# Performance work log

Measured on AMD Instinct MI355X. Metric: run time of the kernel, lower is better.

Reference implementation:

```python
import jax, jax.numpy as jnp
import numpy as np

B, S = 128, 32
V, E, H, L = 32000, 512, 1024, 2


def setup_inputs() -> dict:
    key = jax.random.key(0)
    ks = jax.random.split(key, 16)
    s = 0.02  # weight scale
    inp = {
        "x": jax.random.randint(ks[0], (B, S), 0, V),
        "encoder_output": jax.random.normal(ks[1], (S, B, H), jnp.float32),  # unused by module
        "encoder_hidden_state": jax.random.normal(ks[2], (L, B, H), jnp.float32),
        "emb": jax.random.normal(ks[3], (V, E), jnp.float32) * s,
        "w_ih0": jax.random.normal(ks[4], (3 * H, E), jnp.float32) * s,
        "w_hh0": jax.random.normal(ks[5], (3 * H, H), jnp.float32) * s,
        "b_ih0": jax.random.normal(ks[6], (3 * H,), jnp.float32) * s,
        "b_hh0": jax.random.normal(ks[7], (3 * H,), jnp.float32) * s,
        "w_ih1": jax.random.normal(ks[8], (3 * H, H), jnp.float32) * s,
        "w_hh1": jax.random.normal(ks[9], (3 * H, H), jnp.float32) * s,
        "b_ih1": jax.random.normal(ks[10], (3 * H,), jnp.float32) * s,
        "b_hh1": jax.random.normal(ks[11], (3 * H,), jnp.float32) * s,
        "w_dec": jax.random.normal(ks[12], (V, H), jnp.float32) * s,
        "b_dec": jax.random.normal(ks[13], (V,), jnp.float32) * s,
        "max_seq_length": S,
    }
    return inp


def _gru_cell(h, xt, w_ih, w_hh, b_ih, b_hh):
    # PyTorch GRU gate math
    gi = xt @ w_ih.T + b_ih  # [B, 3H]
    gh = h @ w_hh.T + b_hh   # [B, 3H]
    ir, iz, inn = jnp.split(gi, 3, axis=-1)
    hr, hz, hn = jnp.split(gh, 3, axis=-1)
    r = jax.nn.sigmoid(ir + hr)
    z = jax.nn.sigmoid(iz + hz)
    n = jnp.tanh(inn + r * hn)
    return (1.0 - z) * n + z * h


def reference(x, encoder_output, encoder_hidden_state, emb,
              w_ih0, w_hh0, b_ih0, b_hh0,
              w_ih1, w_hh1, b_ih1, b_hh1,
              w_dec, b_dec, max_seq_length):
    # teaching_rate = 0.0 -> pure teacher forcing; dropout p=0.0 -> identity.
    # Step 0 consumes SOS token (id 1, from torch.ones().long()); steps 1..T-1 consume x[:, i].
    Bsz = x.shape[0]
    sos = jnp.ones((Bsz, 1), jnp.int32)
    toks = jnp.concatenate([sos, x[:, 1:max_seq_length].astype(jnp.int32)], axis=1)  # [B, T]
    xs = emb[toks].transpose(1, 0, 2)  # [T, B, E] (seq-first, matching permute(1,0,2))

    def step(carry, xt):
        h0, h1 = carry
        h0 = _gru_cell(h0, xt, w_ih0, w_hh0, b_ih0, b_hh0)
        h1 = _gru_cell(h1, h0, w_ih1, w_hh1, b_ih1, b_hh1)
        return (h0, h1), h1

    init = (encoder_hidden_state[0], encoder_hidden_state[1])
    _, ys = jax.lax.scan(step, init, xs)  # ys: [T, B, H]
    logits = jnp.einsum('tbh,vh->tbv', ys, w_dec) + b_dec  # [T, B, V]
    return logits
```

## Files before the change

kernel.cpp:

```cpp
#include <hip/hip_runtime.h>
#include <hip/hip_bf16.h>
#include <stdint.h>

#define T_SEQ 32
#define BATCH 128
#define EMB   512
#define HID   1024
#define VOC   32000
#define G3    (3 * HID)
#define MROWS (T_SEQ * BATCH)
#define BHID  (BATCH * HID)

typedef __bf16 bf16_t;
typedef __bf16 bf16x8 __attribute__((ext_vector_type(8)));
typedef __bf16 bf16x4 __attribute__((ext_vector_type(4)));
typedef float  f32x4  __attribute__((ext_vector_type(4)));

#define MFMA(a, b, c) __builtin_amdgcn_mfma_f32_16x16x32_bf16((a), (b), (c), 0, 0, 0)

union U64cast  { bf16x4 v; unsigned long long u; };
union U128cast { f32x4 v; unsigned long long u[2]; };

__device__ __forceinline__ unsigned flag_ld(const unsigned* p) {
    return __hip_atomic_load(p, __ATOMIC_RELAXED, __HIP_MEMORY_SCOPE_SYSTEM);
}
__device__ __forceinline__ void flag_st(unsigned* p, unsigned v) {
    __hip_atomic_store(p, v, __ATOMIC_RELAXED, __HIP_MEMORY_SCOPE_SYSTEM);
}

__global__ void fused_cvt_kernel(
    const float* __restrict__ w_ih0, const float* __restrict__ w_hh0,
    const float* __restrict__ w_ih1, const float* __restrict__ w_hh1,
    const float* __restrict__ w_dec, const float* __restrict__ enc_hid,
    bf16_t* __restrict__ Wih0b, bf16_t* __restrict__ Whh0b,
    bf16_t* __restrict__ Wih1b, bf16_t* __restrict__ Whh1b,
    bf16_t* __restrict__ Wdecb, bf16_t* __restrict__ h0ib,
    bf16_t* __restrict__ h1ib) {
    const int b = blockIdx.x;
    const float* src;
    bf16_t* dst;
    int base;
    if (b < 1536)       { src = w_ih0;          dst = Wih0b; base = b; }
    else if (b < 4608)  { src = w_hh0;          dst = Whh0b; base = b - 1536; }
    else if (b < 7680)  { src = w_ih1;          dst = Wih1b; base = b - 4608; }
    else if (b < 10752) { src = w_hh1;          dst = Whh1b; base = b - 7680; }
    else if (b < 42752) { src = w_dec;          dst = Wdecb; base = b - 10752; }
    else if (b < 42880) { src = enc_hid;        dst = h0ib;  base = b - 42752; }
    else                { src = enc_hid + BHID; dst = h1ib;  base = b - 42880; }
    const int i = base * 1024 + threadIdx.x * 4;
    float4 v = *(const float4*)(src + i);
    dst[i + 0] = (bf16_t)v.x;
    dst[i + 1] = (bf16_t)v.y;
    dst[i + 2] = (bf16_t)v.z;
    dst[i + 3] = (bf16_t)v.w;
}

__global__ void embed_kernel(const int* __restrict__ x,
                             const float* __restrict__ emb,
                             bf16_t* __restrict__ X) {
    int m = blockIdx.x;
    int t = m >> 7, b = m & 127;
    int tok = (t == 0) ? 1 : x[b * T_SEQ + t];
    const float* src = emb + (size_t)tok * EMB;
    bf16_t* dst = X + (size_t)m * EMB;
    int c = threadIdx.x * 4;
    float4 v = *(const float4*)(src + c);
    dst[c + 0] = (bf16_t)v.x;
    dst[c + 1] = (bf16_t)v.y;
    dst[c + 2] = (bf16_t)v.z;
    dst[c + 3] = (bf16_t)v.w;
}

#define GLOAD_LDS16(g, l)                                                    \
    __builtin_amdgcn_global_load_lds(                                        \
        (const __attribute__((address_space(1))) void*)(g),                  \
        (__attribute__((address_space(3))) void*)(l), 16, 0, 0)

template <int BIAS>
__global__ __launch_bounds__(256) void gemm_bf16_kernel(
    const bf16_t* __restrict__ A, const bf16_t* __restrict__ B,
    const float* __restrict__ bias, float* __restrict__ C,
    int M, int N, int K) {
    __shared__ __align__(16) bf16_t As[128 * 32];
    __shared__ __align__(16) bf16_t Bs[128 * 32];

    const int nbm = gridDim.y, nbn = gridDim.x;
    const int nwg = nbm * nbn;
    int lin = blockIdx.y * nbn + blockIdx.x;
    if ((nwg & 7) == 0) {
        int xcd = lin & 7, idx = lin >> 3;
        lin = xcd * (nwg >> 3) + idx;
    }
    const int bm = (lin % nbm) * 128;
    const int bn = (lin / nbm) * 128;

    const int tid  = threadIdx.x;
    const int lane = tid & 63;
    const int w    = tid >> 6;
    const int wr   = w >> 1, wc = w & 1;

    f32x4 acc[4][4] = {};

    const int lrow = tid >> 2;
    const int lcol = (tid & 3) * 8;
    const bf16_t* ag = A + (size_t)(bm + lrow) * K + lcol;
    const bf16_t* bg = B + (size_t)(bn + lrow) * K + lcol;
    bf16_t* asl0 = As + lrow * 32 + lcol;
    bf16_t* asl1 = As + (lrow + 64) * 32 + lcol;
    bf16_t* bsl0 = Bs + lrow * 32 + lcol;
    bf16_t* bsl1 = Bs + (lrow + 64) * 32 + lcol;

    const int r16 = lane & 15;
    const int kh  = (lane >> 4) * 8;

    for (int k0 = 0; k0 < K; k0 += 32) {
        GLOAD_LDS16(ag + k0, asl0);
        GLOAD_LDS16(ag + (size_t)64 * K + k0, asl1);
        GLOAD_LDS16(bg + k0, bsl0);
        GLOAD_LDS16(bg + (size_t)64 * K + k0, bsl1);
        __syncthreads();

        bf16x8 af[4], bf[4];
#pragma unroll
        for (int mi = 0; mi < 4; ++mi)
            af[mi] = *(const bf16x8*)(As + (wr * 64 + mi * 16 + r16) * 32 + kh);
#pragma unroll
        for (int ni = 0; ni < 4; ++ni)
            bf[ni] = *(const bf16x8*)(Bs + (wc * 64 + ni * 16 + r16) * 32 + kh);
#pragma unroll
        for (int mi = 0; mi < 4; ++mi)
#pragma unroll
            for (int ni = 0; ni < 4; ++ni)
                acc[mi][ni] = MFMA(af[mi], bf[ni], acc[mi][ni]);
        __syncthreads();
    }

#pragma unroll
    for (int mi = 0; mi < 4; ++mi) {
        const int row0 = bm + wr * 64 + mi * 16 + (lane >> 4) * 4;
#pragma unroll
        for (int ni = 0; ni < 4; ++ni) {
            const int col = bn + wc * 64 + ni * 16 + r16;
            float bv = 0.f;
            if (BIAS) bv = bias[col];
#pragma unroll
            for (int r = 0; r < 4; ++r)
                C[(size_t)(row0 + r) * N + col] = acc[mi][ni][r] + bv;
        }
    }
}

template <int BIAS>
__global__ __launch_bounds__(512, 1) void gemm256_bf16_kernel(
    const bf16_t* __restrict__ A, const bf16_t* __restrict__ B,
    const float* __restrict__ bias, float* __restrict__ C,
    int M, int N, int K) {
    __shared__ __align__(16) bf16_t lds[2 * 2 * 16384];

    const int NT = K >> 6;
    const int nbm = gridDim.y, nbn = gridDim.x;
    const int nwg = nbm * nbn;
    int lin = blockIdx.y * nbn + blockIdx.x;
    {
        int q = nwg >> 3, r = nwg & 7, x = lin & 7, i = lin >> 3;
        lin = (x < r ? x * (q + 1) : r * (q + 1) + (x - r) * q) + i;
    }
    const int bm = (lin % nbm) * 256;
    const int bn = (lin / nbm) * 256;

    const int tid = threadIdx.x, lane = tid & 63;
    const int w = tid >> 6, wm = w >> 2, wn = w & 3;
    const int r16 = lane & 15, sl = lane >> 4, r7 = r16 & 7;

    const int srow  = tid >> 3;
    const int sslot = (tid & 7) ^ (srow & 7);
    const bf16_t* agS = A + (size_t)(bm + srow) * K + sslot * 8;
    const bf16_t* bgS = B + (size_t)(bn + srow) * K + sslot * 8;

    const int colk0 = ((0 + sl) ^ r7) * 8;
    const int colk1 = ((4 + sl) ^ r7) * 8;
    const int arow = (wm * 128 + r16) * 64;
    const int brow = (wn * 64 + r16) * 64;

    f32x4 acc[8][4] = {};
    bf16x8 af[4][2], bf[4][2];

#pragma unroll
    for (int l = 0; l < 4; ++l)
        GLOAD_LDS16(agS + (size_t)(l * 64) * K, lds + l * 4096 + tid * 8);
#pragma unroll
    for (int l = 0; l < 4; ++l)
        GLOAD_LDS16(bgS + (size_t)(l * 64) * K, lds + 16384 + l * 4096 + tid * 8);
#pragma unroll
    for (int l = 0; l < 4; ++l)
        GLOAD_LDS16(agS + (size_t)(l * 64) * K + 64,
                    lds + 32768 + l * 4096 + tid * 8);
#pragma unroll
    for (int l = 0; l < 4; ++l)
        GLOAD_LDS16(bgS + (size_t)(l * 64) * K + 64,
                    lds + 49152 + l * 4096 + tid * 8);
    asm volatile("s_waitcnt vmcnt(8)" ::: "memory");
    __builtin_amdgcn_sched_barrier(0);
    __builtin_amdgcn_s_barrier();

#pragma unroll 1
    for (int kt = 0; kt < NT; ++kt) {
        const int cur = kt & 1;
        const bf16_t* Ab = lds + cur * 32768;
        const bf16_t* Bb = Ab + 16384;
        bf16_t* Sb = lds + cur * 32768;
        const bool st = (kt + 2 < NT);
        const size_t kof = (size_t)(kt + 2) * 64;

#pragma unroll
        for (int fr = 0; fr < 4; ++fr) {
            af[fr][0] = *(const bf16x8*)(Ab + arow + fr * 1024 + colk0);
            af[fr][1] = *(const bf16x8*)(Ab + arow + fr * 1024 + colk1);
        }
#pragma unroll
        for (int nf = 0; nf < 2; ++nf) {
            bf[nf][0] = *(const bf16x8*)(Bb + brow + nf * 1024 + colk0);
            bf[nf][1] = *(const bf16x8*)(Bb + brow + nf * 1024 + colk1);
        }
        __builtin_amdgcn_sched_barrier(0);
        __builtin_amdgcn_s_barrier();
        asm volatile("s_waitcnt lgkmcnt(0)" ::: "memory");
        __builtin_amdgcn_sched_barrier(0);
        __builtin_amdgcn_s_setprio(1);
#pragma unroll
        for (int fr = 0; fr < 4; ++fr)
#pragma unroll
            for (int nf = 0; nf < 2; ++nf) {
                acc[fr][nf] = MFMA(af[fr][0], bf[nf][0], acc[fr][nf]);
                acc[fr][nf] = MFMA(af[fr][1], bf[nf][1], acc[fr][nf]);
            }
        __builtin_amdgcn_s_setprio(0);
        __builtin_amdgcn_sched_barrier(0);
        __builtin_amdgcn_s_barrier();

#pragma unroll
        for (int nf = 2; nf < 4; ++nf) {
            bf[nf][0] = *(const bf16x8*)(Bb + brow + nf * 1024 + colk0);
            bf[nf][1] = *(const bf16x8*)(Bb + brow + nf * 1024 + colk1);
        }
        __builtin_amdgcn_sched_barrier(0);
        if (st) {
            GLOAD_LDS16(agS + kof, Sb + tid * 8);
            GLOAD_LDS16(agS + (size_t)128 * K + kof, Sb + 8192 + tid * 8);
        }
        __builtin_amdgcn_s_barrier();
        asm volatile("s_waitcnt lgkmcnt(0)" ::: "memory");
        __builtin_amdgcn_sched_barrier(0);
        __builtin_amdgcn_s_setprio(1);
#pragma unroll
        for (int fr = 0; fr < 4; ++fr)
#pragma unroll
            for (int nf = 2; nf < 4; ++nf) {
                acc[fr][nf] = MFMA(af[fr][0], bf[nf][0], acc[fr][nf]);
                acc[fr][nf] = MFMA(af[fr][1], bf[nf][1], acc[fr][nf]);
            }
        __builtin_amdgcn_s_setprio(0);
        __builtin_amdgcn_sched_barrier(0);
        __builtin_amdgcn_s_barrier();

#pragma unroll
        for (int fr = 0; fr < 4; ++fr) {
            af[fr][0] = *(const bf16x8*)(Ab + arow + (fr + 4) * 1024 + colk0);
            af[fr][1] = *(const bf16x8*)(Ab + arow + (fr + 4) * 1024 + colk1);
        }
        __builtin_amdgcn_sched_barrier(0);
        if (st) {
#pragma unroll
            for (int l = 0; l < 4; ++l)
                GLOAD_LDS16(bgS + (size_t)(l * 64) * K + kof,
                            Sb + 16384 + l * 4096 + tid * 8);
        }
        __builtin_amdgcn_s_barrier();
        asm volatile("s_waitcnt lgkmcnt(0)" ::: "memory");
        __builtin_amdgcn_sched_barrier(0);
        __builtin_amdgcn_s_setprio(1);
#pragma unroll
        for (int fr = 0; fr < 4; ++fr)
#pragma unroll
            for (int nf = 0; nf < 2; ++nf) {
                acc[fr + 4][nf] = MFMA(af[fr][0], bf[nf][0], acc[fr + 4][nf]);
                acc[fr + 4][nf] = MFMA(af[fr][1], bf[nf][1], acc[fr + 4][nf]);
            }
        __builtin_amdgcn_s_setprio(0);
        __builtin_amdgcn_sched_barrier(0);
        __builtin_amdgcn_s_barrier();

        if (st) {
            GLOAD_LDS16(agS + (size_t)64 * K + kof, Sb + 4096 + tid * 8);
            GLOAD_LDS16(agS + (size_t)192 * K + kof, Sb + 12288 + tid * 8);
        }
        if (kt + 2 < NT) {
            asm volatile("s_waitcnt vmcnt(8)" ::: "memory");
        } else if (kt + 1 < NT) {
            asm volatile("s_waitcnt vmcnt(0)" ::: "memory");
        }
        __builtin_amdgcn_sched_barrier(0);
        __builtin_amdgcn_s_setprio(1);
#pragma unroll
        for (int fr = 0; fr < 4; ++fr)
#pragma unroll
            for (int nf = 2; nf < 4; ++nf) {
                acc[fr + 4][nf] = MFMA(af[fr][0], bf[nf][0], acc[fr + 4][nf]);
                acc[fr + 4][nf] = MFMA(af[fr][1], bf[nf][1], acc[fr + 4][nf]);
            }
        __builtin_amdgcn_s_setprio(0);
        __builtin_amdgcn_sched_barrier(0);
        __builtin_amdgcn_s_barrier();
    }

#pragma unroll
    for (int fr = 0; fr < 8; ++fr) {
        const int row0 = bm + wm * 128 + fr * 16 + sl * 4;
#pragma unroll
        for (int nf = 0; nf < 4; ++nf) {
            const int col = bn + wn * 64 + nf * 16 + r16;
            float bv = 0.f;
            if (BIAS) bv = bias[col];
#pragma unroll
            for (int r = 0; r < 4; ++r)
                __builtin_nontemporal_store(
                    acc[fr][nf][r] + bv, &C[(size_t)(row0 + r) * N + col]);
        }
    }
}

__global__ __launch_bounds__(256, 1) void fused_scan_kernel(
    const bf16_t* __restrict__ h0ib, const bf16_t* __restrict__ h1ib,
    const float* __restrict__ enc_hid,
    const bf16_t* __restrict__ whh0, const bf16_t* __restrict__ wih1,
    const bf16_t* __restrict__ whh1,
    const float* __restrict__ bhh0, const float* __restrict__ bih1,
    const float* __restrict__ bhh1,
    float* __restrict__ Gi, bf16_t* __restrict__ H0b,
    bf16_t* __restrict__ H1b, unsigned* __restrict__ wfl) {
    __shared__ __align__(16) float Sg[4][3][128][16];

    const int tid  = threadIdx.x;
    const int lane = tid & 63;
    const int w    = tid >> 6;
    const int role = blockIdx.x >> 6;
    const int cb   = blockIdx.x & 63;
    const int c0   = cb * 16;
    const int r16  = lane & 15;
    const int kq   = (lane >> 4) * 8;

    const int FL0 = 0, FG = 256, FL1 = 512;

    const bf16_t* whh = role == 0 ? whh0 : (role == 1 ? wih1 : whh1);
    const float*  bia = role == 0 ? bhh0 : (role == 1 ? bih1 : bhh1);

    bf16x8 wf[3][8];
#pragma unroll
    for (int g = 0; g < 3; ++g)
#pragma unroll
        for (int kf = 0; kf < 8; ++kf)
            wf[g][kf] = *(const bf16x8*)(
                whh + (size_t)(g * HID + c0 + r16) * HID + w * 256 + kf * 32 + kq);

    const int cg   = tid & 3;
    const int rloc = tid >> 2;
    const int ce   = c0 + cg * 4;

    float bh[3][4];
#pragma unroll
    for (int g = 0; g < 3; ++g)
#pragma unroll
        for (int j = 0; j < 4; ++j) bh[g][j] = bia[g * HID + ce + j];

    float hp[2][4];
    if (role != 1) {
        const float* h0f = enc_hid + (role == 2 ? BHID : 0);
#pragma unroll
        for (int i = 0; i < 2; ++i)
#pragma unroll
            for (int j = 0; j < 4; ++j)
                hp[i][j] = h0f[(size_t)(rloc + i * 64) * HID + ce + j];
    }

    f32x4 gi[2][3];
    if (role == 0) {
#pragma unroll
        for (int i = 0; i < 2; ++i) {
            const size_t gb = (size_t)(rloc + i * 64) * G3 + ce;
            gi[i][0] = *(const f32x4*)(Gi + gb);
            gi[i][1] = *(const f32x4*)(Gi + gb + HID);
            gi[i][2] = *(const f32x4*)(Gi + gb + 2 * HID);
        }
    }

    for (int t = 0; t < T_SEQ; ++t) {
        if (role == 0) {
            if (t && tid < 64) {
#pragma unroll
                for (int j = 0; j < 4; ++j)
                    while (flag_ld(&wfl[FL0 + tid * 4 + j]) < (unsigned)t)
                        __builtin_amdgcn_s_sleep(1);
            }
        } else if (role == 1) {
            if (tid < 64) {
#pragma unroll
                for (int j = 0; j < 4; ++j)
                    while (flag_ld(&wfl[FL0 + tid * 4 + j]) < (unsigned)(t + 1))
                        __builtin_amdgcn_s_sleep(1);
            }
        } else {
            if (tid < 64) {
                if (t) {
#pragma unroll
                    for (int j = 0; j < 4; ++j)
                        while (flag_ld(&wfl[FL1 + tid * 4 + j]) < (unsigned)t)
                            __builtin_amdgcn_s_sleep(1);
                }
            } else if (tid < 68) {
                while (flag_ld(&wfl[FG + cb * 4 + (tid - 64)]) <
                       (unsigned)(t + 1))
                    __builtin_amdgcn_s_sleep(1);
            }
        }
        __syncthreads();

        if (role == 2) {
#pragma unroll
            for (int i = 0; i < 2; ++i) {
                const size_t gb =
                    ((size_t)t * BATCH + rloc + i * 64) * G3 + ce;
#pragma unroll
                for (int g = 0; g < 3; ++g) {
                    U128cast u;
                    const unsigned long long* p =
                        (const unsigned long long*)(Gi + gb + g * HID);
                    u.u[0] = __hip_atomic_load(p, __ATOMIC_RELAXED,
                                               __HIP_MEMORY_SCOPE_SYSTEM);
                    u.u[1] = __hip_atomic_load(p + 1, __ATOMIC_RELAXED,
                                               __HIP_MEMORY_SCOPE_SYSTEM);
                    gi[i][g] = u.v;
                }
            }
        }

        const bf16_t* hb =
            role == 0 ? (t ? H0b + (size_t)(t - 1) * BHID : h0ib)
          : role == 1 ? (H0b + (size_t)t * BHID)
                      : (t ? H1b + (size_t)(t - 1) * BHID : h1ib);

        f32x4 acc[3][8] = {};
        bf16x8 af[4][8];
#define LD_GROUP(buf, kf)                                                    \
    {                                                                        \
        const int kbase = w * 256 + (kf) * 32 + kq;                          \
        _Pragma("unroll") for (int rf = 0; rf < 8; ++rf)                     \
            af[buf][rf] =                                                    \
                *(const bf16x8*)(hb + (size_t)(rf * 16 + r16) * HID + kbase); \
    }
        LD_GROUP(0, 0)
        LD_GROUP(1, 1)
        LD_GROUP(2, 2)
#pragma unroll
        for (int kf = 0; kf < 8; ++kf) {
            if (kf + 3 < 8) LD_GROUP((kf + 3) & 3, kf + 3)
#pragma unroll
            for (int rf = 0; rf < 8; ++rf) {
                acc[0][rf] = MFMA(af[kf & 3][rf], wf[0][kf], acc[0][rf]);
                acc[1][rf] = MFMA(af[kf & 3][rf], wf[1][kf], acc[1][rf]);
                acc[2][rf] = MFMA(af[kf & 3][rf], wf[2][kf], acc[2][rf]);
            }
        }
#undef LD_GROUP

#pragma unroll
        for (int g = 0; g < 3; ++g)
#pragma unroll
            for (int rf = 0; rf < 8; ++rf)
#pragma unroll
                for (int r = 0; r < 4; ++r)
                    Sg[w][g][rf * 16 + (lane >> 4) * 4 + r][r16] = acc[g][rf][r];
        __syncthreads();

#pragma unroll
        for (int i = 0; i < 2; ++i) {
            const int row = rloc + i * 64;
            f32x4 gr = *(const f32x4*)&Sg[0][0][row][cg * 4];
            f32x4 gz = *(const f32x4*)&Sg[0][1][row][cg * 4];
            f32x4 gn = *(const f32x4*)&Sg[0][2][row][cg * 4];
#pragma unroll
            for (int ks = 1; ks < 4; ++ks) {
                gr += *(const f32x4*)&Sg[ks][0][row][cg * 4];
                gz += *(const f32x4*)&Sg[ks][1][row][cg * 4];
                gn += *(const f32x4*)&Sg[ks][2][row][cg * 4];
            }
            if (role == 1) {
                const size_t gb = ((size_t)t * BATCH + row) * G3 + ce;
                U128cast s0, s1, s2;
#pragma unroll
                for (int j = 0; j < 4; ++j) {
                    s0.v[j] = gr[j] + bh[0][j];
                    s1.v[j] = gz[j] + bh[1][j];
                    s2.v[j] = gn[j] + bh[2][j];
                }
                unsigned long long* p0 = (unsigned long long*)(Gi + gb);
                unsigned long long* p1 = (unsigned long long*)(Gi + gb + HID);
                unsigned long long* p2 = (unsigned long long*)(Gi + gb + 2 * HID);
                __hip_atomic_store(p0, s0.u[0], __ATOMIC_RELAXED, __HIP_MEMORY_SCOPE_SYSTEM);
                __hip_atomic_store(p0 + 1, s0.u[1], __ATOMIC_RELAXED, __HIP_MEMORY_SCOPE_SYSTEM);
                __hip_atomic_store(p1, s1.u[0], __ATOMIC_RELAXED, __HIP_MEMORY_SCOPE_SYSTEM);
                __hip_atomic_store(p1 + 1, s1.u[1], __ATOMIC_RELAXED, __HIP_MEMORY_SCOPE_SYSTEM);
                __hip_atomic_store(p2, s2.u[0], __ATOMIC_RELAXED, __HIP_MEMORY_SCOPE_SYSTEM);
                __hip_atomic_store(p2 + 1, s2.u[1], __ATOMIC_RELAXED, __HIP_MEMORY_SCOPE_SYSTEM);
            } else {
                U64cast hb4;
#pragma unroll
                for (int j = 0; j < 4; ++j) {
                    float rr = 1.f / (1.f + __expf(-(gi[i][0][j] + gr[j] + bh[0][j])));
                    float zz = 1.f / (1.f + __expf(-(gi[i][1][j] + gz[j] + bh[1][j])));
                    float nn = tanhf(gi[i][2][j] + rr * (gn[j] + bh[2][j]));
                    float h  = (1.f - zz) * nn + zz * hp[i][j];
                    hp[i][j] = h;
                    hb4.v[j] = (bf16_t)h;
                }
                bf16_t* dst = (role == 0 ? H0b : H1b) +
                              (size_t)t * BHID + (size_t)row * HID + ce;
                __hip_atomic_store((unsigned long long*)dst, hb4.u,
                                   __ATOMIC_RELAXED, __HIP_MEMORY_SCOPE_SYSTEM);
            }
        }

        asm volatile("s_waitcnt vmcnt(0)" ::: "memory");
        __builtin_amdgcn_sched_barrier(0);
        if (lane == 0)
            flag_st(&wfl[role * 256 + cb * 4 + w], (unsigned)(t + 1));

        if (role == 0 && t + 1 < T_SEQ) {
#pragma unroll
            for (int i = 0; i < 2; ++i) {
                const size_t gb =
                    ((size_t)(t + 1) * BATCH + rloc + i * 64) * G3 + ce;
                gi[i][0] = *(const f32x4*)(Gi + gb);
                gi[i][1] = *(const f32x4*)(Gi + gb + HID);
                gi[i][2] = *(const f32x4*)(Gi + gb + 2 * HID);
            }
        }
        __syncthreads();
    }
}

extern "C" void kernel_launch(void* const* d_in, const int* in_sizes, int n_in,
                              void* d_out, int out_size, void* d_ws, size_t ws_size,
                              hipStream_t stream) {
    const int*   x        = (const int*)d_in[0];
    const float* enc_hid  = (const float*)d_in[2];
    const float* emb      = (const float*)d_in[3];
    const float* w_ih0    = (const float*)d_in[4];
    const float* w_hh0    = (const float*)d_in[5];
    const float* b_ih0    = (const float*)d_in[6];
    const float* b_hh0    = (const float*)d_in[7];
    const float* w_ih1    = (const float*)d_in[8];
    const float* w_hh1    = (const float*)d_in[9];
    const float* b_ih1    = (const float*)d_in[10];
    const float* b_hh1    = (const float*)d_in[11];
    const float* w_dec    = (const float*)d_in[12];
    const float* b_dec    = (const float*)d_in[13];
    float* out = (float*)d_out;

    char* ws = (char*)d_ws;
    size_t off = 0;
    auto alloc = [&](size_t bytes) {
        void* p = ws + off;
        off += (bytes + 255) & ~(size_t)255;
        return p;
    };
    unsigned* wfl  = (unsigned*)alloc(4096);
    bf16_t* Xb     = (bf16_t*)alloc((size_t)MROWS * EMB * 2);
    bf16_t* Wih0b  = (bf16_t*)alloc((size_t)G3 * EMB * 2);
    bf16_t* Whh0b  = (bf16_t*)alloc((size_t)G3 * HID * 2);
    bf16_t* Wih1b  = (bf16_t*)alloc((size_t)G3 * HID * 2);
    bf16_t* Whh1b  = (bf16_t*)alloc((size_t)G3 * HID * 2);
    bf16_t* Wdecb  = (bf16_t*)alloc((size_t)VOC * HID * 2);
    bf16_t* h0ib   = (bf16_t*)alloc((size_t)BATCH * HID * 2);
    bf16_t* h1ib   = (bf16_t*)alloc((size_t)BATCH * HID * 2);
    float*  Gi     = (float*)alloc((size_t)MROWS * G3 * 4);
    bf16_t* H0b    = (bf16_t*)alloc((size_t)MROWS * HID * 2);
    bf16_t* H1b    = (bf16_t*)alloc((size_t)MROWS * HID * 2);

    hipMemsetAsync(wfl, 0, 4096, stream);

    fused_cvt_kernel<<<43008, 256, 0, stream>>>(
        w_ih0, w_hh0, w_ih1, w_hh1, w_dec, enc_hid,
        Wih0b, Whh0b, Wih1b, Whh1b, Wdecb, h0ib, h1ib);

    embed_kernel<<<MROWS, 128, 0, stream>>>(x, emb, Xb);

    gemm_bf16_kernel<1><<<dim3(G3 / 128, MROWS / 128), 256, 0, stream>>>(
        Xb, Wih0b, b_ih0, Gi, MROWS, G3, EMB);

    fused_scan_kernel<<<192, 256, 0, stream>>>(
        h0ib, h1ib, enc_hid, Whh0b, Wih1b, Whh1b,
        b_hh0, b_ih1, b_hh1, Gi, H0b, H1b, wfl);

    gemm256_bf16_kernel<1><<<dim3(VOC / 256, MROWS / 256), 512, 0, stream>>>(
        H1b, Wdecb, b_dec, out, MROWS, VOC, HID);
}
```

Baseline: 906.7 us.

## Fuse decoder GEMM into scan kernel with work-stealing tiles overlapping recurrence

Removes the separate 256x256 decoder GEMM and launches 448 blocks. The first 192 blocks run the GRU recurrence, and every block then pulls 128x128 output tiles from an atomic counter. Each tile waits on the per-timestep layer-1 flags, so vocabulary projection for finished timesteps overlaps the sequential scan instead of waiting for it to end. The trade-off is a simpler single-buffered 128x128 GEMM with no double buffering, which may lose throughput compared with the tuned 256 kernel. Extra co-resident blocks could also slow the latency-critical scan, so the scan section raises its wave priority and shrinks its LDS staging to bf16 to make room for the GEMM buffers.

```diff
diff --git a/kernel.cpp b/kernel.cpp
--- a/kernel.cpp
+++ b/kernel.cpp
@@ -10,6 +10,7 @@
 #define G3    (3 * HID)
 #define MROWS (T_SEQ * BATCH)
 #define BHID  (BATCH * HID)
+#define NTILE 8000
 
 typedef __bf16 bf16_t;
 typedef __bf16 bf16x8 __attribute__((ext_vector_type(8)));
@@ -150,186 +151,7 @@
     }
 }
 
-template <int BIAS>
-__global__ __launch_bounds__(512, 1) void gemm256_bf16_kernel(
-    const bf16_t* __restrict__ A, const bf16_t* __restrict__ B,
-    const float* __restrict__ bias, float* __restrict__ C,
-    int M, int N, int K) {
-    __shared__ __align__(16) bf16_t lds[2 * 2 * 16384];
-
-    const int NT = K >> 6;
-    const int nbm = gridDim.y, nbn = gridDim.x;
-    const int nwg = nbm * nbn;
-    int lin = blockIdx.y * nbn + blockIdx.x;
-    {
-        int q = nwg >> 3, r = nwg & 7, x = lin & 7, i = lin >> 3;
-        lin = (x < r ? x * (q + 1) : r * (q + 1) + (x - r) * q) + i;
-    }
-    const int bm = (lin % nbm) * 256;
-    const int bn = (lin / nbm) * 256;
-
-    const int tid = threadIdx.x, lane = tid & 63;
-    const int w = tid >> 6, wm = w >> 2, wn = w & 3;
-    const int r16 = lane & 15, sl = lane >> 4, r7 = r16 & 7;
-
-    const int srow  = tid >> 3;
-    const int sslot = (tid & 7) ^ (srow & 7);
-    const bf16_t* agS = A + (size_t)(bm + srow) * K + sslot * 8;
-    const bf16_t* bgS = B + (size_t)(bn + srow) * K + sslot * 8;
-
-    const int colk0 = ((0 + sl) ^ r7) * 8;
-    const int colk1 = ((4 + sl) ^ r7) * 8;
-    const int arow = (wm * 128 + r16) * 64;
-    const int brow = (wn * 64 + r16) * 64;
-
-    f32x4 acc[8][4] = {};
-    bf16x8 af[4][2], bf[4][2];
-
-#pragma unroll
-    for (int l = 0; l < 4; ++l)
-        GLOAD_LDS16(agS + (size_t)(l * 64) * K, lds + l * 4096 + tid * 8);
-#pragma unroll
-    for (int l = 0; l < 4; ++l)
-        GLOAD_LDS16(bgS + (size_t)(l * 64) * K, lds + 16384 + l * 4096 + tid * 8);
-#pragma unroll
-    for (int l = 0; l < 4; ++l)
-        GLOAD_LDS16(agS + (size_t)(l * 64) * K + 64,
-                    lds + 32768 + l * 4096 + tid * 8);
-#pragma unroll
-    for (int l = 0; l < 4; ++l)
-        GLOAD_LDS16(bgS + (size_t)(l * 64) * K + 64,
-                    lds + 49152 + l * 4096 + tid * 8);
-    asm volatile("s_waitcnt vmcnt(8)" ::: "memory");
-    __builtin_amdgcn_sched_barrier(0);
-    __builtin_amdgcn_s_barrier();
-
-#pragma unroll 1
-    for (int kt = 0; kt < NT; ++kt) {
-        const int cur = kt & 1;
-        const bf16_t* Ab = lds + cur * 32768;
-        const bf16_t* Bb = Ab + 16384;
-        bf16_t* Sb = lds + cur * 32768;
-        const bool st = (kt + 2 < NT);
-        const size_t kof = (size_t)(kt + 2) * 64;
-
-#pragma unroll
-        for (int fr = 0; fr < 4; ++fr) {
-            af[fr][0] = *(const bf16x8*)(Ab + arow + fr * 1024 + colk0);
-            af[fr][1] = *(const bf16x8*)(Ab + arow + fr * 1024 + colk1);
-        }
-#pragma unroll
-        for (int nf = 0; nf < 2; ++nf) {
-            bf[nf][0] = *(const bf16x8*)(Bb + brow + nf * 1024 + colk0);
-            bf[nf][1] = *(const bf16x8*)(Bb + brow + nf * 1024 + colk1);
-        }
-        __builtin_amdgcn_sched_barrier(0);
-        __builtin_amdgcn_s_barrier();
-        asm volatile("s_waitcnt lgkmcnt(0)" ::: "memory");
-        __builtin_amdgcn_sched_barrier(0);
-        __builtin_amdgcn_s_setprio(1);
-#pragma unroll
-        for (int fr = 0; fr < 4; ++fr)
-#pragma unroll
-            for (int nf = 0; nf < 2; ++nf) {
-                acc[fr][nf] = MFMA(af[fr][0], bf[nf][0], acc[fr][nf]);
-                acc[fr][nf] = MFMA(af[fr][1], bf[nf][1], acc[fr][nf]);
-            }
-        __builtin_amdgcn_s_setprio(0);
-        __builtin_amdgcn_sched_barrier(0);
-        __builtin_amdgcn_s_barrier();
-
-#pragma unroll
-        for (int nf = 2; nf < 4; ++nf) {
-            bf[nf][0] = *(const bf16x8*)(Bb + brow + nf * 1024 + colk0);
-            bf[nf][1] = *(const bf16x8*)(Bb + brow + nf * 1024 + colk1);
-        }
-        __builtin_amdgcn_sched_barrier(0);
-        if (st) {
-            GLOAD_LDS16(agS + kof, Sb + tid * 8);
-            GLOAD_LDS16(agS + (size_t)128 * K + kof, Sb + 8192 + tid * 8);
-        }
-        __builtin_amdgcn_s_barrier();
-        asm volatile("s_waitcnt lgkmcnt(0)" ::: "memory");
-        __builtin_amdgcn_sched_barrier(0);
-        __builtin_amdgcn_s_setprio(1);
-#pragma unroll
-        for (int fr = 0; fr < 4; ++fr)
-#pragma unroll
-            for (int nf = 2; nf < 4; ++nf) {
-                acc[fr][nf] = MFMA(af[fr][0], bf[nf][0], acc[fr][nf]);
-                acc[fr][nf] = MFMA(af[fr][1], bf[nf][1], acc[fr][nf]);
-            }
-        __builtin_amdgcn_s_setprio(0);
-        __builtin_amdgcn_sched_barrier(0);
-        __builtin_amdgcn_s_barrier();
-
-#pragma unroll
-        for (int fr = 0; fr < 4; ++fr) {
-            af[fr][0] = *(const bf16x8*)(Ab + arow + (fr + 4) * 1024 + colk0);
-            af[fr][1] = *(const bf16x8*)(Ab + arow + (fr + 4) * 1024 + colk1);
-        }
-        __builtin_amdgcn_sched_barrier(0);
-        if (st) {
-#pragma unroll
-            for (int l = 0; l < 4; ++l)
-                GLOAD_LDS16(bgS + (size_t)(l * 64) * K + kof,
-                            Sb + 16384 + l * 4096 + tid * 8);
-        }
-        __builtin_amdgcn_s_barrier();
-        asm volatile("s_waitcnt lgkmcnt(0)" ::: "memory");
-        __builtin_amdgcn_sched_barrier(0);
-        __builtin_amdgcn_s_setprio(1);
-#pragma unroll
-        for (int fr = 0; fr < 4; ++fr)
-#pragma unroll
-            for (int nf = 0; nf < 2; ++nf) {
-                acc[fr + 4][nf] = MFMA(af[fr][0], bf[nf][0], acc[fr + 4][nf]);
-                acc[fr + 4][nf] = MFMA(af[fr][1], bf[nf][1], acc[fr + 4][nf]);
-            }
-        __builtin_amdgcn_s_setprio(0);
-        __builtin_amdgcn_sched_barrier(0);
-        __builtin_amdgcn_s_barrier();
-
-        if (st) {
-            GLOAD_LDS16(agS + (size_t)64 * K + kof, Sb + 4096 + tid * 8);
-            GLOAD_LDS16(agS + (size_t)192 * K + kof, Sb + 12288 + tid * 8);
-        }
-        if (kt + 2 < NT) {
-            asm volatile("s_waitcnt vmcnt(8)" ::: "memory");
-        } else if (kt + 1 < NT) {
-            asm volatile("s_waitcnt vmcnt(0)" ::: "memory");
-        }
-        __builtin_amdgcn_sched_barrier(0);
-        __builtin_amdgcn_s_setprio(1);
-#pragma unroll
-        for (int fr = 0; fr < 4; ++fr)
-#pragma unroll
-            for (int nf = 2; nf < 4; ++nf) {
-                acc[fr + 4][nf] = MFMA(af[fr][0], bf[nf][0], acc[fr + 4][nf]);
-                acc[fr + 4][nf] = MFMA(af[fr][1], bf[nf][1], acc[fr + 4][nf]);
-            }
-        __builtin_amdgcn_s_setprio(0);
-        __builtin_amdgcn_sched_barrier(0);
-        __builtin_amdgcn_s_barrier();
-    }
-
-#pragma unroll
-    for (int fr = 0; fr < 8; ++fr) {
-        const int row0 = bm + wm * 128 + fr * 16 + sl * 4;
-#pragma unroll
-        for (int nf = 0; nf < 4; ++nf) {
-            const int col = bn + wn * 64 + nf * 16 + r16;
-            float bv = 0.f;
-            if (BIAS) bv = bias[col];
-#pragma unroll
-            for (int r = 0; r < 4; ++r)
-                __builtin_nontemporal_store(
-                    acc[fr][nf][r] + bv, &C[(size_t)(row0 + r) * N + col]);
-        }
-    }
-}
-
-__global__ __launch_bounds__(256, 1) void fused_scan_kernel(
+__global__ __launch_bounds__(256, 1) void scan_steal_kernel(
     const bf16_t* __restrict__ h0ib, const bf16_t* __restrict__ h1ib,
     const float* __restrict__ enc_hid,
     const bf16_t* __restrict__ whh0, const bf16_t* __restrict__ wih1,
@@ -337,119 +159,128 @@
     const float* __restrict__ bhh0, const float* __restrict__ bih1,
     const float* __restrict__ bhh1,
     float* __restrict__ Gi, bf16_t* __restrict__ H0b,
-    bf16_t* __restrict__ H1b, unsigned* __restrict__ wfl) {
-    __shared__ __align__(16) float Sg[4][3][128][16];
+    bf16_t* __restrict__ H1b,
+    const bf16_t* __restrict__ Wdecb, const float* __restrict__ bdec,
+    float* __restrict__ out, unsigned* __restrict__ wfl) {
+    __shared__ __align__(16) bf16_t SgB[4][3][128][16];
+    __shared__ unsigned tileShared;
 
     const int tid  = threadIdx.x;
     const int lane = tid & 63;
-    const int w    = tid >> 6;
-    const int role = blockIdx.x >> 6;
-    const int cb   = blockIdx.x & 63;
-    const int c0   = cb * 16;
-    const int r16  = lane & 15;
-    const int kq   = (lane >> 4) * 8;
-
+    const int bid  = blockIdx.x;
     const int FL0 = 0, FG = 256, FL1 = 512;
 
-    const bf16_t* whh = role == 0 ? whh0 : (role == 1 ? wih1 : whh1);
-    const float*  bia = role == 0 ? bhh0 : (role == 1 ? bih1 : bhh1);
-
-    bf16x8 wf[3][8];
-#pragma unroll
-    for (int g = 0; g < 3; ++g)
-#pragma unroll
-        for (int kf = 0; kf < 8; ++kf)
-            wf[g][kf] = *(const bf16x8*)(
-                whh + (size_t)(g * HID + c0 + r16) * HID + w * 256 + kf * 32 + kq);
-
-    const int cg   = tid & 3;
-    const int rloc = tid >> 2;
-    const int ce   = c0 + cg * 4;
-
-    float bh[3][4];
-#pragma unroll
-    for (int g = 0; g < 3; ++g)
-#pragma unroll
-        for (int j = 0; j < 4; ++j) bh[g][j] = bia[g * HID + ce + j];
-
-    float hp[2][4];
-    if (role != 1) {
-        const float* h0f = enc_hid + (role == 2 ? BHID : 0);
-#pragma unroll
-        for (int i = 0; i < 2; ++i)
-#pragma unroll
-            for (int j = 0; j < 4; ++j)
-                hp[i][j] = h0f[(size_t)(rloc + i * 64) * HID + ce + j];
-    }
-
-    f32x4 gi[2][3];
-    if (role == 0) {
-#pragma unroll
-        for (int i = 0; i < 2; ++i) {
-            const size_t gb = (size_t)(rloc + i * 64) * G3 + ce;
-            gi[i][0] = *(const f32x4*)(Gi + gb);
-            gi[i][1] = *(const f32x4*)(Gi + gb + HID);
-            gi[i][2] = *(const f32x4*)(Gi + gb + 2 * HID);
+    if (bid < 192) {
+        const int w    = tid >> 6;
+        const int role = bid >> 6;
+        const int cb   = bid & 63;
+        const int c0   = cb * 16;
+        const int r16  = lane & 15;
+        const int kq   = (lane >> 4) * 8;
+
+        const bf16_t* whh = role == 0 ? whh0 : (role == 1 ? wih1 : whh1);
+        const float*  bia = role == 0 ? bhh0 : (role == 1 ? bih1 : bhh1);
+
+        bf16x8 wf[3][8];
+#pragma unroll
+        for (int g = 0; g < 3; ++g)
+#pragma unroll
+            for (int kf = 0; kf < 8; ++kf)
+                wf[g][kf] = *(const bf16x8*)(
+                    whh + (size_t)(g * HID + c0 + r16) * HID + w * 256 +
+                    kf * 32 + kq);
+
+        const int cg   = tid & 3;
+        const int rloc = tid >> 2;
+        const int ce   = c0 + cg * 4;
+
+        float bh[3][4];
+#pragma unroll
+        for (int g = 0; g < 3; ++g)
+#pragma unroll
+            for (int j = 0; j < 4; ++j) bh[g][j] = bia[g * HID + ce + j];
+
+        float hp[2][4];
+        if (role != 1) {
+            const float* h0f = enc_hid + (role == 2 ? BHID : 0);
+#pragma unroll
+            for (int i = 0; i < 2; ++i)
+#pragma unroll
+                for (int j = 0; j < 4; ++j)
+                    hp[i][j] = h0f[(size_t)(rloc + i * 64) * HID + ce + j];
         }
-    }
-
-    for (int t = 0; t < T_SEQ; ++t) {
+
+        f32x4 gi[2][3];
         if (role == 0) {
-            if (t && tid < 64) {
-#pragma unroll
-                for (int j = 0; j < 4; ++j)
-                    while (flag_ld(&wfl[FL0 + tid * 4 + j]) < (unsigned)t)
+#pragma unroll
+            for (int i = 0; i < 2; ++i) {
+                const size_t gb = (size_t)(rloc + i * 64) * G3 + ce;
+                gi[i][0] = *(const f32x4*)(Gi + gb);
+                gi[i][1] = *(const f32x4*)(Gi + gb + HID);
+                gi[i][2] = *(const f32x4*)(Gi + gb + 2 * HID);
+            }
+        }
+
+        for (int t = 0; t < T_SEQ; ++t) {
+            if (role == 0) {
+                if (t && tid < 64) {
+#pragma unroll
+                    for (int j = 0; j < 4; ++j)
+                        while (flag_ld(&wfl[FL0 + tid * 4 + j]) < (unsigned)t)
+                            __builtin_amdgcn_s_sleep(1);
+                }
+            } else if (role == 1) {
+                if (tid < 64) {
+#pragma unroll
+                    for (int j = 0; j < 4; ++j)
+                        while (flag_ld(&wfl[FL0 + tid * 4 + j]) <
+                               (unsigned)(t + 1))
+                            __builtin_amdgcn_s_sleep(1);
+                }
+            } else {
+                if (tid < 64) {
+                    if (t) {
+#pragma unroll
+                        for (int j = 0; j < 4; ++j)
+                            while (flag_ld(&wfl[FL1 + tid * 4 + j]) <
+                                   (unsigned)t)
+                                __builtin_amdgcn_s_sleep(1);
+                    }
+                } else if (tid < 68) {
+                    while (flag_ld(&wfl[FG + cb * 4 + (tid - 64)]) <
+                           (unsigned)(t + 1))
                         __builtin_amdgcn_s_sleep(1);
-            }
-        } else if (role == 1) {
-            if (tid < 64) {
-#pragma unroll
-                for (int j = 0; j < 4; ++j)
-                    while (flag_ld(&wfl[FL0 + tid * 4 + j]) < (unsigned)(t + 1))
-                        __builtin_amdgcn_s_sleep(1);
-            }
-        } else {
-            if (tid < 64) {
-                if (t) {
-#pragma unroll
-                    for (int j = 0; j < 4; ++j)
-                        while (flag_ld(&wfl[FL1 + tid * 4 + j]) < (unsigned)t)
-                            __builtin_amdgcn_s_sleep(1);
-                }
-            } else if (tid < 68) {
-                while (flag_ld(&wfl[FG + cb * 4 + (tid - 64)]) <
-                       (unsigned)(t + 1))
-                    __builtin_amdgcn_s_sleep(1);
-            }
-        }
-        __syncthreads();
-
-        if (role == 2) {
-#pragma unroll
-            for (int i = 0; i < 2; ++i) {
-                const size_t gb =
-                    ((size_t)t * BATCH + rloc + i * 64) * G3 + ce;
-#pragma unroll
-                for (int g = 0; g < 3; ++g) {
-                    U128cast u;
-                    const unsigned long long* p =
-                        (const unsigned long long*)(Gi + gb + g * HID);
-                    u.u[0] = __hip_atomic_load(p, __ATOMIC_RELAXED,
-                                               __HIP_MEMORY_SCOPE_SYSTEM);
-                    u.u[1] = __hip_atomic_load(p + 1, __ATOMIC_RELAXED,
-                                               __HIP_MEMORY_SCOPE_SYSTEM);
-                    gi[i][g] = u.v;
-                }
-            }
-        }
-
-        const bf16_t* hb =
-            role == 0 ? (t ? H0b + (size_t)(t - 1) * BHID : h0ib)
-          : role == 1 ? (H0b + (size_t)t * BHID)
-                      : (t ? H1b + (size_t)(t - 1) * BHID : h1ib);
-
-        f32x4 acc[3][8] = {};
-        bf16x8 af[4][8];
+                }
+            }
+            __syncthreads();
+            __builtin_amdgcn_s_setprio(1);
+
+            if (role == 2) {
+#pragma unroll
+                for (int i = 0; i < 2; ++i) {
+                    const size_t gb =
+                        ((size_t)t * BATCH + rloc + i * 64) * G3 + ce;
+#pragma unroll
+                    for (int g = 0; g < 3; ++g) {
+                        U128cast u;
+                        const unsigned long long* p =
+                            (const unsigned long long*)(Gi + gb + g * HID);
+                        u.u[0] = __hip_atomic_load(p, __ATOMIC_RELAXED,
+                                                   __HIP_MEMORY_SCOPE_SYSTEM);
+                        u.u[1] = __hip_atomic_load(p + 1, __ATOMIC_RELAXED,
+                                                   __HIP_MEMORY_SCOPE_SYSTEM);
+                        gi[i][g] = u.v;
+                    }
+                }
+            }
+
+            const bf16_t* hb =
+                role == 0 ? (t ? H0b + (size_t)(t - 1) * BHID : h0ib)
+              : role == 1 ? (H0b + (size_t)t * BHID)
+                          : (t ? H1b + (size_t)(t - 1) * BHID : h1ib);
+
+            f32x4 acc[3][8] = {};
+            bf16x8 af[4][8];
 #define LD_GROUP(buf, kf)                                                    \
     {                                                                        \
         const int kbase = w * 256 + (kf) * 32 + kq;                          \
@@ -457,94 +288,180 @@
             af[buf][rf] =                                                    \
                 *(const bf16x8*)(hb + (size_t)(rf * 16 + r16) * HID + kbase); \
     }
-        LD_GROUP(0, 0)
-        LD_GROUP(1, 1)
-        LD_GROUP(2, 2)
-#pragma unroll
-        for (int kf = 0; kf < 8; ++kf) {
-            if (kf + 3 < 8) LD_GROUP((kf + 3) & 3, kf + 3)
-#pragma unroll
-            for (int rf = 0; rf < 8; ++rf) {
-                acc[0][rf] = MFMA(af[kf & 3][rf], wf[0][kf], acc[0][rf]);
-                acc[1][rf] = MFMA(af[kf & 3][rf], wf[1][kf], acc[1][rf]);
-                acc[2][rf] = MFMA(af[kf & 3][rf], wf[2][kf], acc[2][rf]);
-            }
+            LD_GROUP(0, 0)
+            LD_GROUP(1, 1)
+            LD_GROUP(2, 2)
+#pragma unroll
+            for (int kf = 0; kf < 8; ++kf) {
+                if (kf + 3 < 8) LD_GROUP((kf + 3) & 3, kf + 3)
+#pragma unroll
+                for (int rf = 0; rf < 8; ++rf) {
+                    acc[0][rf] = MFMA(af[kf & 3][rf], wf[0][kf], acc[0][rf]);
+                    acc[1][rf] = MFMA(af[kf & 3][rf], wf[1][kf], acc[1][rf]);
+                    acc[2][rf] = MFMA(af[kf & 3][rf], wf[2][kf], acc[2][rf]);
+                }
+            }
+#undef LD_GROUP
+
+#pragma unroll
+            for (int g = 0; g < 3; ++g)
+#pragma unroll
+                for (int rf = 0; rf < 8; ++rf)
+#pragma unroll
+                    for (int r = 0; r < 4; ++r)
+                        SgB[w][g][rf * 16 + (lane >> 4) * 4 + r][r16] =
+                            (bf16_t)acc[g][rf][r];
+            __syncthreads();
+
+#pragma unroll
+            for (int i = 0; i < 2; ++i) {
+                const int row = rloc + i * 64;
+                float gr[4] = {0, 0, 0, 0}, gz[4] = {0, 0, 0, 0},
+                      gn[4] = {0, 0, 0, 0};
+#pragma unroll
+                for (int ks = 0; ks < 4; ++ks) {
+                    bf16x4 vr = *(const bf16x4*)&SgB[ks][0][row][cg * 4];
+                    bf16x4 vz = *(const bf16x4*)&SgB[ks][1][row][cg * 4];
+                    bf16x4 vn = *(const bf16x4*)&SgB[ks][2][row][cg * 4];
+#pragma unroll
+                    for (int j = 0; j < 4; ++j) {
+                        gr[j] += (float)vr[j];
+                        gz[j] += (float)vz[j];
+                        gn[j] += (float)vn[j];
+                    }
+                }
+                if (role == 1) {
+                    const size_t gb = ((size_t)t * BATCH + row) * G3 + ce;
+                    U128cast s0, s1, s2;
+#pragma unroll
+                    for (int j = 0; j < 4; ++j) {
+                        s0.v[j] = gr[j] + bh[0][j];
+                        s1.v[j] = gz[j] + bh[1][j];
+                        s2.v[j] = gn[j] + bh[2][j];
+                    }
+                    unsigned long long* p0 = (unsigned long long*)(Gi + gb);
+                    unsigned long long* p1 = (unsigned long long*)(Gi + gb + HID);
+                    unsigned long long* p2 = (unsigned long long*)(Gi + gb + 2 * HID);
+                    __hip_atomic_store(p0, s0.u[0], __ATOMIC_RELAXED, __HIP_MEMORY_SCOPE_SYSTEM);
+                    __hip_atomic_store(p0 + 1, s0.u[1], __ATOMIC_RELAXED, __HIP_MEMORY_SCOPE_SYSTEM);
+                    __hip_atomic_store(p1, s1.u[0], __ATOMIC_RELAXED, __HIP_MEMORY_SCOPE_SYSTEM);
+                    __hip_atomic_store(p1 + 1, s1.u[1], __ATOMIC_RELAXED, __HIP_MEMORY_SCOPE_SYSTEM);
+                    __hip_atomic_store(p2, s2.u[0], __ATOMIC_RELAXED, __HIP_MEMORY_SCOPE_SYSTEM);
+                    __hip_atomic_store(p2 + 1, s2.u[1], __ATOMIC_RELAXED, __HIP_MEMORY_SCOPE_SYSTEM);
+                } else {
+                    U64cast hb4;
+#pragma unroll
+                    for (int j = 0; j < 4; ++j) {
+                        float rr = 1.f / (1.f + __expf(-(gi[i][0][j] + gr[j] + bh[0][j])));
+                        float zz = 1.f / (1.f + __expf(-(gi[i][1][j] + gz[j] + bh[1][j])));
+                        float nn = tanhf(gi[i][2][j] + rr * (gn[j] + bh[2][j]));
+                        float h  = (1.f - zz) * nn + zz * hp[i][j];
+                        hp[i][j] = h;
+                        hb4.v[j] = (bf16_t)h;
+                    }
+                    bf16_t* dst = (role == 0 ? H0b : H1b) +
+                                  (size_t)t * BHID + (size_t)row * HID + ce;
+                    __hip_atomic_store((unsigned long long*)dst, hb4.u,
+                                       __ATOMIC_RELAXED,
+                                       __HIP_MEMORY_SCOPE_SYSTEM);
+                }
+            }
+
+            asm volatile("s_waitcnt vmcnt(0)" ::: "memory");
+            __builtin_amdgcn_sched_barrier(0);
+            if (lane == 0)
+                flag_st(&wfl[role * 256 + cb * 4 + w], (unsigned)(t + 1));
+            __builtin_amdgcn_s_setprio(0);
+
+            if (role == 0 && t + 1 < T_SEQ) {
+#pragma unroll
+                for (int i = 0; i < 2; ++i) {
+                    const size_t gb =
+                        ((size_t)(t + 1) * BATCH + rloc + i * 64) * G3 + ce;
+                    gi[i][0] = *(const f32x4*)(Gi + gb);
+                    gi[i][1] = *(const f32x4*)(Gi + gb + HID);
+                    gi[i][2] = *(const f32x4*)(Gi + gb + 2 * HID);
+                }
+            }
+            __syncthreads();
         }
-#undef LD_GROUP
-
-#pragma unroll
-        for (int g = 0; g < 3; ++g)
-#pragma unroll
-            for (int rf = 0; rf < 8; ++rf)
-#pragma unroll
-                for (int r = 0; r < 4; ++r)
-                    Sg[w][g][rf * 16 + (lane >> 4) * 4 + r][r16] = acc[g][rf][r];
-        __syncthreads();
-
-#pragma unroll
-        for (int i = 0; i < 2; ++i) {
-            const int row = rloc + i * 64;
-            f32x4 gr = *(const f32x4*)&Sg[0][0][row][cg * 4];
-            f32x4 gz = *(const f32x4*)&Sg[0][1][row][cg * 4];
-            f32x4 gn = *(const f32x4*)&Sg[0][2][row][cg * 4];
-#pragma unroll
-            for (int ks = 1; ks < 4; ++ks) {
-                gr += *(const f32x4*)&Sg[ks][0][row][cg * 4];
-                gz += *(const f32x4*)&Sg[ks][1][row][cg * 4];
-                gn += *(const f32x4*)&Sg[ks][2][row][cg * 4];
-            }
-            if (role == 1) {
-                const size_t gb = ((size_t)t * BATCH + row) * G3 + ce;
-                U128cast s0, s1, s2;
-#pragma unroll
-                for (int j = 0; j < 4; ++j) {
-                    s0.v[j] = gr[j] + bh[0][j];
-                    s1.v[j] = gz[j] + bh[1][j];
-                    s2.v[j] = gn[j] + bh[2][j];
-                }
-                unsigned long long* p0 = (unsigned long long*)(Gi + gb);
-                unsigned long long* p1 = (unsigned long long*)(Gi + gb + HID);
-                unsigned long long* p2 = (unsigned long long*)(Gi + gb + 2 * HID);
-                __hip_atomic_store(p0, s0.u[0], __ATOMIC_RELAXED, __HIP_MEMORY_SCOPE_SYSTEM);
-                __hip_atomic_store(p0 + 1, s0.u[1], __ATOMIC_RELAXED, __HIP_MEMORY_SCOPE_SYSTEM);
-                __hip_atomic_store(p1, s1.u[0], __ATOMIC_RELAXED, __HIP_MEMORY_SCOPE_SYSTEM);
-                __hip_atomic_store(p1 + 1, s1.u[1], __ATOMIC_RELAXED, __HIP_MEMORY_SCOPE_SYSTEM);
-                __hip_atomic_store(p2, s2.u[0], __ATOMIC_RELAXED, __HIP_MEMORY_SCOPE_SYSTEM);
-                __hip_atomic_store(p2 + 1, s2.u[1], __ATOMIC_RELAXED, __HIP_MEMORY_SCOPE_SYSTEM);
-            } else {
-                U64cast hb4;
-#pragma unroll
-                for (int j = 0; j < 4; ++j) {
-                    float rr = 1.f / (1.f + __expf(-(gi[i][0][j] + gr[j] + bh[0][j])));
-                    float zz = 1.f / (1.f + __expf(-(gi[i][1][j] + gz[j] + bh[1][j])));
-                    float nn = tanhf(gi[i][2][j] + rr * (gn[j] + bh[2][j]));
-                    float h  = (1.f - zz) * nn + zz * hp[i][j];
-                    hp[i][j] = h;
-                    hb4.v[j] = (bf16_t)h;
-                }
-                bf16_t* dst = (role == 0 ? H0b : H1b) +
-                              (size_t)t * BHID + (size_t)row * HID + ce;
-                __hip_atomic_store((unsigned long long*)dst, hb4.u,
-                                   __ATOMIC_RELAXED, __HIP_MEMORY_SCOPE_SYSTEM);
+    }
+
+    {
+        bf16_t* As = (bf16_t*)SgB;
+        bf16_t* Bs = As + 128 * 32;
+        unsigned* ctr = wfl + 768;
+        const int w4 = tid >> 6, wr = w4 >> 1, wc = w4 & 1;
+        const int lrow = tid >> 2, lcol = (tid & 3) * 8;
+        const int r16 = lane & 15, kh = (lane >> 4) * 8;
+
+        int have = 0;
+        for (;;) {
+            __syncthreads();
+            if (tid == 0)
+                tileShared = __hip_atomic_fetch_add(ctr, 1u, __ATOMIC_RELAXED,
+                                                    __HIP_MEMORY_SCOPE_AGENT);
+            __syncthreads();
+            const int tile = (int)tileShared;
+            if (tile >= NTILE) break;
+
+            const int rt = tile / 250, ct = tile - rt * 250;
+            const int bm = rt * 128, bn = ct * 128;
+            if (rt + 1 > have) {
+                if (tid < 64) {
+#pragma unroll
+                    for (int j = 0; j < 4; ++j)
+                        while (flag_ld(&wfl[512 + tid * 4 + j]) <
+                               (unsigned)(rt + 1))
+                            __builtin_amdgcn_s_sleep(16);
+                }
+                __syncthreads();
+                have = rt + 1;
+            }
+
+            const bf16_t* ag = H1b + (size_t)(bm + lrow) * HID + lcol;
+            const bf16_t* bg = Wdecb + (size_t)(bn + lrow) * HID + lcol;
+            f32x4 acc[4][4] = {};
+
+            for (int k0 = 0; k0 < HID; k0 += 32) {
+                GLOAD_LDS16(ag + k0, As + lrow * 32 + lcol);
+                GLOAD_LDS16(ag + (size_t)64 * HID + k0,
+                            As + (lrow + 64) * 32 + lcol);
+                GLOAD_LDS16(bg + k0, Bs + lrow * 32 + lcol);
+                GLOAD_LDS16(bg + (size_t)64 * HID + k0,
+                            Bs + (lrow + 64) * 32 + lcol);
+                __syncthreads();
+
+                bf16x8 af[4], bf[4];
+#pragma unroll
+                for (int mi = 0; mi < 4; ++mi)
+                    af[mi] = *(const bf16x8*)(As + (wr * 64 + mi * 16 + r16) * 32 + kh);
+#pragma unroll
+                for (int ni = 0; ni < 4; ++ni)
+                    bf[ni] = *(const bf16x8*)(Bs + (wc * 64 + ni * 16 + r16) * 32 + kh);
+#pragma unroll
+                for (int mi = 0; mi < 4; ++mi)
+#pragma unroll
+                    for (int ni = 0; ni < 4; ++ni)
+                        acc[mi][ni] = MFMA(af[mi], bf[ni], acc[mi][ni]);
+                __syncthreads();
+            }
+
+#pragma unroll
+            for (int mi = 0; mi < 4; ++mi) {
+                const int row0 = bm + wr * 64 + mi * 16 + (lane >> 4) * 4;
+#pragma unroll
+                for (int ni = 0; ni < 4; ++ni) {
+                    const int col = bn + wc * 64 + ni * 16 + r16;
+                    const float bv = bdec[col];
+#pragma unroll
+                    for (int r = 0; r < 4; ++r)
+                        __builtin_nontemporal_store(
+                            acc[mi][ni][r] + bv,
+                            &out[(size_t)(row0 + r) * VOC + col]);
+                }
             }
         }
-
-        asm volatile("s_waitcnt vmcnt(0)" ::: "memory");
-        __builtin_amdgcn_sched_barrier(0);
-        if (lane == 0)
-            flag_st(&wfl[role * 256 + cb * 4 + w], (unsigned)(t + 1));
-
-        if (role == 0 && t + 1 < T_SEQ) {
-#pragma unroll
-            for (int i = 0; i < 2; ++i) {
-                const size_t gb =
-                    ((size_t)(t + 1) * BATCH + rloc + i * 64) * G3 + ce;
-                gi[i][0] = *(const f32x4*)(Gi + gb);
-                gi[i][1] = *(const f32x4*)(Gi + gb + HID);
-                gi[i][2] = *(const f32x4*)(Gi + gb + 2 * HID);
-            }
-        }
-        __syncthreads();
     }
 }
 
@@ -597,10 +514,8 @@
     gemm_bf16_kernel<1><<<dim3(G3 / 128, MROWS / 128), 256, 0, stream>>>(
         Xb, Wih0b, b_ih0, Gi, MROWS, G3, EMB);
 
-    fused_scan_kernel<<<192, 256, 0, stream>>>(
+    scan_steal_kernel<<<448, 256, 0, stream>>>(
         h0ib, h1ib, enc_hid, Whh0b, Wih1b, Whh1b,
-        b_hh0, b_ih1, b_hh1, Gi, H0b, H1b, wfl);
-
-    gemm256_bf16_kernel<1><<<dim3(VOC / 256, MROWS / 256), 512, 0, stream>>>(
-        H1b, Wdecb, b_dec, out, MROWS, VOC, HID);
-}
+        b_hh0, b_ih1, b_hh1, Gi, H0b, H1b,
+        Wdecb, b_dec, out, wfl);
+}
```

After: 1.128 ms. 1.24x slower.

## Overlap decoder weight bf16 conversion with the recurrent scan kernel

Applied to the files above, without the earlier changes.

Moves the fp32-to-bf16 conversion of the large decoder weight matrix out of the upfront conversion kernel and into 64 extra blocks of the persistent scan kernel. Those blocks convert w_dec while the 192 scan blocks run their latency-bound recurrence, so the conversion bandwidth is meant to hide behind the scan. The risk is that the converter blocks compete for memory bandwidth and CUs with the scan. Co-residency is also a concern: the scan blocks spin on flags, so if they cannot all be resident alongside the converter blocks the scan could stall.

```diff
diff --git a/kernel.cpp b/kernel.cpp
--- a/kernel.cpp
+++ b/kernel.cpp
@@ -31,11 +31,10 @@
 __global__ void fused_cvt_kernel(
     const float* __restrict__ w_ih0, const float* __restrict__ w_hh0,
     const float* __restrict__ w_ih1, const float* __restrict__ w_hh1,
-    const float* __restrict__ w_dec, const float* __restrict__ enc_hid,
+    const float* __restrict__ enc_hid,
     bf16_t* __restrict__ Wih0b, bf16_t* __restrict__ Whh0b,
     bf16_t* __restrict__ Wih1b, bf16_t* __restrict__ Whh1b,
-    bf16_t* __restrict__ Wdecb, bf16_t* __restrict__ h0ib,
-    bf16_t* __restrict__ h1ib) {
+    bf16_t* __restrict__ h0ib, bf16_t* __restrict__ h1ib) {
     const int b = blockIdx.x;
     const float* src;
     bf16_t* dst;
@@ -44,9 +43,8 @@
     else if (b < 4608)  { src = w_hh0;          dst = Whh0b; base = b - 1536; }
     else if (b < 7680)  { src = w_ih1;          dst = Wih1b; base = b - 4608; }
     else if (b < 10752) { src = w_hh1;          dst = Whh1b; base = b - 7680; }
-    else if (b < 42752) { src = w_dec;          dst = Wdecb; base = b - 10752; }
-    else if (b < 42880) { src = enc_hid;        dst = h0ib;  base = b - 42752; }
-    else                { src = enc_hid + BHID; dst = h1ib;  base = b - 42880; }
+    else if (b < 10880) { src = enc_hid;        dst = h0ib;  base = b - 10752; }
+    else                { src = enc_hid + BHID; dst = h1ib;  base = b - 10880; }
     const int i = base * 1024 + threadIdx.x * 4;
     float4 v = *(const float4*)(src + i);
     dst[i + 0] = (bf16_t)v.x;
@@ -337,14 +335,32 @@
     const float* __restrict__ bhh0, const float* __restrict__ bih1,
     const float* __restrict__ bhh1,
     float* __restrict__ Gi, bf16_t* __restrict__ H0b,
-    bf16_t* __restrict__ H1b, unsigned* __restrict__ wfl) {
+    bf16_t* __restrict__ H1b, unsigned* __restrict__ wfl,
+    const float* __restrict__ wdec_f, bf16_t* __restrict__ Wdecb) {
     __shared__ __align__(16) float Sg[4][3][128][16];
 
     const int tid  = threadIdx.x;
+    const int bid  = blockIdx.x;
+
+    if (bid >= 192) {
+        const int cvtid = (bid - 192) * 256 + tid;
+#pragma unroll 4
+        for (int it = 0; it < 500; ++it) {
+            const size_t i = ((size_t)it * 16384 + cvtid) * 4;
+            float4 v = *(const float4*)(wdec_f + i);
+            bf16_t* d = Wdecb + i;
+            d[0] = (bf16_t)v.x;
+            d[1] = (bf16_t)v.y;
+            d[2] = (bf16_t)v.z;
+            d[3] = (bf16_t)v.w;
+        }
+        return;
+    }
+
     const int lane = tid & 63;
     const int w    = tid >> 6;
-    const int role = blockIdx.x >> 6;
-    const int cb   = blockIdx.x & 63;
+    const int role = bid >> 6;
+    const int cb   = bid & 63;
     const int c0   = cb * 16;
     const int r16  = lane & 15;
     const int kq   = (lane >> 4) * 8;
@@ -588,18 +604,18 @@
 
     hipMemsetAsync(wfl, 0, 4096, stream);
 
-    fused_cvt_kernel<<<43008, 256, 0, stream>>>(
-        w_ih0, w_hh0, w_ih1, w_hh1, w_dec, enc_hid,
-        Wih0b, Whh0b, Wih1b, Whh1b, Wdecb, h0ib, h1ib);
+    fused_cvt_kernel<<<11008, 256, 0, stream>>>(
+        w_ih0, w_hh0, w_ih1, w_hh1, enc_hid,
+        Wih0b, Whh0b, Wih1b, Whh1b, h0ib, h1ib);
 
     embed_kernel<<<MROWS, 128, 0, stream>>>(x, emb, Xb);
 
     gemm_bf16_kernel<1><<<dim3(G3 / 128, MROWS / 128), 256, 0, stream>>>(
         Xb, Wih0b, b_ih0, Gi, MROWS, G3, EMB);
 
-    fused_scan_kernel<<<192, 256, 0, stream>>>(
+    fused_scan_kernel<<<256, 256, 0, stream>>>(
         h0ib, h1ib, enc_hid, Whh0b, Wih1b, Whh1b,
-        b_hh0, b_ih1, b_hh1, Gi, H0b, H1b, wfl);
+        b_hh0, b_ih1, b_hh1, Gi, H0b, H1b, wfl, w_dec, Wdecb);
 
     gemm256_bf16_kernel<1><<<dim3(VOC / 256, MROWS / 256), 512, 0, stream>>>(
         H1b, Wdecb, b_dec, out, MROWS, VOC, HID);
```

Measured after the change: 878.6 us. 3.1% less time.
